# Performance work log

Measured on AMD Instinct MI355X. Metric: run time of the kernel, lower is better.

Reference implementation:

```python
import jax, jax.numpy as jnp
import numpy as np

N_NODES = 100000
N_EDGES = 1600000


def setup_inputs() -> dict:
    key = jax.random.key(0)
    k1, k2, k3, k4, k5, k6 = jax.random.split(key, 6)
    x = jax.random.normal(k1, (N_NODES, 2), dtype=jnp.float32)
    edge_index = jax.random.randint(k2, (2, N_EDGES), 0, N_NODES, dtype=jnp.int64)
    # Glorot-style init for GCN weights, zeros for biases (PyG defaults)
    W1 = jax.random.normal(k3, (2, 64), dtype=jnp.float32) * (1.0 / np.sqrt(2.0))
    b1 = jnp.zeros((64,), dtype=jnp.float32)
    W2 = jax.random.normal(k4, (64, 1), dtype=jnp.float32) * (1.0 / np.sqrt(64.0))
    b2 = jnp.zeros((1,), dtype=jnp.float32)
    return {"x": x, "edge_index": edge_index, "W1": W1, "b1": b1, "W2": W2, "b2": b2}


def reference(x, edge_index, W1, b1, W2, b2):
    N = x.shape[0]
    row, col = edge_index[0], edge_index[1]  # source, target (PyG flow source_to_target)
    # symmetric GCN normalization, degrees from target index (no self loops)
    deg = jax.ops.segment_sum(jnp.ones(edge_index.shape[1], x.dtype), col, num_segments=N)
    deg_inv_sqrt = jnp.where(deg > 0, jnp.where(deg > 0, deg, 1.0) ** -0.5, 0.0)
    norm = (deg_inv_sqrt[row] * deg_inv_sqrt[col])[:, None]  # [E,1]

    def gcn_conv(h, W, b):
        h = h @ W                       # [N,F_out] tiny GEMM
        msg = h[row] * norm             # gather + scale: [E,F_out]
        agg = jax.ops.segment_sum(msg, col, num_segments=N)  # scatter-add
        return agg + b

    h = jax.nn.relu(gcn_conv(x, W1, b1))   # dropout is identity in eval mode
    out = jax.nn.relu(gcn_conv(h, W2, b2))
    return out
```

## Files before the change

### kernel.cpp

```cpp
#include <hip/hip_runtime.h>
#include <math.h>

#define NN 100000
#define NE 1600000
#define BSHIFT 8
#define BKT 256
#define NB 391
#define NBP 392
#define EPB 4096
#define NPB 391
#define STRIDE 5120
#define RT 1024

__global__ void __launch_bounds__(RT) reorder_kernel(
        const int* __restrict__ row, const int* __restrict__ col,
        unsigned* __restrict__ cursor, unsigned* __restrict__ packed) {
    __shared__ int h[NBP], lb[NBP], gb[NBP];
    __shared__ int wsum[RT / 64];
    __shared__ unsigned st[EPB];
    __shared__ unsigned short sbkt[EPB];
    const int t = threadIdx.x;
    const int lane = t & 63, wid = t >> 6;
    const int e0 = blockIdx.x * EPB;
    const int n = min(EPB, NE - e0);

    for (int i = t; i < NBP; i += RT) h[i] = 0;
    __syncthreads();

    const int4* rv = (const int4*)(row + e0);
    const int4* cv = (const int4*)(col + e0);
    unsigned pk[4]; int bb[4];
#pragma unroll
    for (int u = 0; u < 4; ++u) bb[u] = -1;
    if (4 * t < n) {
        int4 r4 = rv[t], c4 = cv[t];
        int rr[4] = {r4.x, r4.y, r4.z, r4.w};
        int cc[4] = {c4.x, c4.y, c4.z, c4.w};
#pragma unroll
        for (int j = 0; j < 4; ++j) {
            pk[j] = ((unsigned)rr[j] << BSHIFT) | (unsigned)(cc[j] & (BKT - 1));
            bb[j] = cc[j] >> BSHIFT;
        }
    }
#pragma unroll
    for (int u = 0; u < 4; ++u)
        if (bb[u] >= 0) atomicAdd(&h[bb[u]], 1);
    __syncthreads();

    int v = (t < NBP) ? h[t] : 0;
    int incl = v;
#pragma unroll
    for (int d = 1; d < 64; d <<= 1) {
        int u = __shfl_up(incl, d);
        if (lane >= d) incl += u;
    }
    if (lane == 63) wsum[wid] = incl;
    __syncthreads();
    int off = 0;
#pragma unroll
    for (int j = 0; j < RT / 64 - 1; ++j)
        if (j < wid) off += wsum[j];
    if (t < NB) {
        lb[t] = off + incl - v;
        gb[t] = v ? (int)atomicAdd(&cursor[t], (unsigned)v) : 0;
    }
    __syncthreads();
    for (int i = t; i < NBP; i += RT) h[i] = 0;
    __syncthreads();

#pragma unroll
    for (int u = 0; u < 4; ++u) {
        if (bb[u] >= 0) {
            int r = atomicAdd(&h[bb[u]], 1);
            int idx = lb[bb[u]] + r;
            st[idx] = pk[u];
            sbkt[idx] = (unsigned short)bb[u];
        }
    }
    __syncthreads();
    for (int i = t; i < n; i += RT) {
        int b = sbkt[i];
        int pos = gb[b] + (i - lb[b]);
        if (pos < STRIDE)
            packed[b * STRIDE + pos] = st[i];
    }
}

__global__ void __launch_bounds__(RT) sortb_kernel(
        const unsigned* __restrict__ packed, const unsigned* __restrict__ cursor,
        const float2* __restrict__ x2,
        unsigned* __restrict__ srow, int2* __restrict__ node_rng,
        float* __restrict__ dis, float2* __restrict__ y2) {
    __shared__ int cnt[BKT], rk[BKT], sexA[BKT];
    __shared__ int wsum[RT / 64];
    __shared__ unsigned st[STRIDE];
    __shared__ unsigned srt[STRIDE];
    const int t = threadIdx.x;
    const int lane = t & 63, wid = t >> 6;
    const int b = blockIdx.x;
    const int s0 = b * STRIDE;
    const int L = min((int)cursor[b], STRIDE);
    const int L4 = L >> 2;

    if (t < BKT) { cnt[t] = 0; rk[t] = 0; }
    __syncthreads();

    const uint4* pv4 = (const uint4*)(packed + s0);
    for (int g = t; g < L4; g += RT) {
        uint4 p4 = pv4[g];
        ((uint4*)st)[g] = p4;
        atomicAdd(&cnt[p4.x & (BKT - 1u)], 1);
        atomicAdd(&cnt[p4.y & (BKT - 1u)], 1);
        atomicAdd(&cnt[p4.z & (BKT - 1u)], 1);
        atomicAdd(&cnt[p4.w & (BKT - 1u)], 1);
    }
    for (int i = 4 * L4 + t; i < L; i += RT) {
        unsigned p = packed[s0 + i];
        st[i] = p;
        atomicAdd(&cnt[p & (BKT - 1u)], 1);
    }
    __syncthreads();

    int v = (t < BKT) ? cnt[t] : 0;
    int incl = v;
#pragma unroll
    for (int d = 1; d < 64; d <<= 1) {
        int u = __shfl_up(incl, d);
        if (lane >= d) incl += u;
    }
    if (lane == 63 && wid < BKT / 64) wsum[wid] = incl;
    __syncthreads();
    int off = 0;
#pragma unroll
    for (int j = 0; j < BKT / 64 - 1; ++j)
        if (j < wid) off += wsum[j];
    if (t < BKT) {
        int sex = off + incl - v;
        sexA[t] = sex;
        int node = (b << BSHIFT) + t;
        if (node < NN) {
            float dv = (v > 0) ? rsqrtf((float)v) : 0.0f;
            dis[node] = dv;
            float2 xv = x2[node];
            y2[node] = make_float2(xv.x * dv, xv.y * dv);
            node_rng[node] = make_int2(s0 + sex, s0 + sex + v);
        }
    }
    __syncthreads();

    for (int i = t; i < L; i += RT) {
        unsigned p = st[i];
        int cl = p & (BKT - 1u);
        int r = atomicAdd(&rk[cl], 1);
        srt[sexA[cl] + r] = p >> BSHIFT;
    }
    __syncthreads();
    uint4* so4 = (uint4*)(srow + s0);
    for (int g = t; g < L4; g += RT) so4[g] = ((const uint4*)srt)[g];
    for (int i = 4 * L4 + t; i < L; i += RT) srow[s0 + i] = srt[i];
}

__global__ void conv1_kernel(const unsigned* __restrict__ srow, const int2* __restrict__ node_rng,
                             const float2* __restrict__ y2, const float* __restrict__ dis,
                             const float* __restrict__ W1, const float* __restrict__ b1,
                             const float* __restrict__ W2, float* __restrict__ z2) {
    __shared__ float sW0[64], sW1[64], sb1[64], sW2[64];
    int t = threadIdx.x;
    if (t < 64) { sW0[t] = W1[t]; sW1[t] = W1[64 + t]; sb1[t] = b1[t]; sW2[t] = W2[t]; }
    __syncthreads();
    int lane = t & 3;
    int node = blockIdx.x * 64 + (t >> 2);
    if (node >= NN) return;
    int2 rng = node_rng[node];
    float sx = 0.f, sy = 0.f;
    for (int k = rng.x + lane; k < rng.y; k += 4) {
        float2 v = y2[srow[k]];
        sx += v.x; sy += v.y;
    }
    sx += __shfl_xor(sx, 1); sy += __shfl_xor(sy, 1);
    sx += __shfl_xor(sx, 2); sy += __shfl_xor(sy, 2);
    float dv = dis[node];
    float a0 = sx * dv, a1 = sy * dv;
    float acc = 0.0f;
    int j0 = lane * 16;
#pragma unroll
    for (int jj = 0; jj < 16; ++jj) {
        int j = j0 + jj;
        float h = fmaf(a0, sW0[j], fmaf(a1, sW1[j], sb1[j]));
        acc = fmaf(fmaxf(h, 0.0f), sW2[j], acc);
    }
    acc += __shfl_xor(acc, 1);
    acc += __shfl_xor(acc, 2);
    if (lane == 0) z2[node] = acc * dv;
}

__global__ void conv2_kernel(const unsigned* __restrict__ srow, const int2* __restrict__ node_rng,
                             const float* __restrict__ z2, const float* __restrict__ dis,
                             const float* __restrict__ b2, float* __restrict__ out) {
    int t = threadIdx.x;
    int lane = t & 3;
    int node = blockIdx.x * 64 + (t >> 2);
    if (node >= NN) return;
    int2 rng = node_rng[node];
    float s = 0.f;
    for (int k = rng.x + lane; k < rng.y; k += 4)
        s += z2[srow[k]];
    s += __shfl_xor(s, 1);
    s += __shfl_xor(s, 2);
    if (lane == 0)
        out[node] = fmaxf(fmaf(dis[node], s, b2[0]), 0.0f);
}

extern "C" void kernel_launch(void* const* d_in, const int* in_sizes, int n_in,
                              void* d_out, int out_size, void* d_ws, size_t ws_size,
                              hipStream_t stream) {
    const float* x  = (const float*)d_in[0];
    const int*   ei = (const int*)d_in[1];
    const float* W1 = (const float*)d_in[2];
    const float* b1 = (const float*)d_in[3];
    const float* W2 = (const float*)d_in[4];
    const float* b2 = (const float*)d_in[5];
    float* out = (float*)d_out;

    const int* row = ei;
    const int* col = ei + NE;

    unsigned* packed   = (unsigned*)d_ws;
    unsigned* srow     = packed + (size_t)NB * STRIDE;
    float2*   y2       = (float2*)(srow + (size_t)NB * STRIDE);
    float*    dis      = (float*)(y2 + NN);
    float*    z2       = dis + NN;
    int2*     node_rng = (int2*)(z2 + NN);
    unsigned* cursor   = (unsigned*)(node_rng + NN);

    hipMemsetAsync(cursor, 0, NB * sizeof(unsigned), stream);

    reorder_kernel<<<NPB, RT, 0, stream>>>(row, col, cursor, packed);
    sortb_kernel  <<<NB, RT, 0, stream>>>(packed, cursor, (const float2*)x,
                                          srow, node_rng, dis, y2);
    conv1_kernel  <<<(NN + 63) / 64, 256, 0, stream>>>(srow, node_rng, y2, dis,
                                                       W1, b1, W2, z2);
    conv2_kernel  <<<(NN + 63) / 64, 256, 0, stream>>>(srow, node_rng, z2, dis, b2, out);
}
```

Before: 117.6 us.

## Use larger 448-node buckets, direct-address scatter staging, and re-read packed in sort

The bucket width grows from 256 to 448 nodes, which cuts the bucket count to 224. Each reorder block now handles 6400 edges with 8 per thread, and per-edge global addresses are precomputed into shared memory so the scatter pass writes directly. The sort kernel no longer stages packed data in LDS and instead re-reads it from global memory for the second pass. Together these aim to reduce block count, per-block fixed overhead and LDS pressure, at the cost of integer division, larger shared arrays and a second global read.

```diff
diff --git a/kernel.cpp b/kernel.cpp
--- a/kernel.cpp
+++ b/kernel.cpp
@@ -3,86 +3,90 @@
 
 #define NN 100000
 #define NE 1600000
-#define BSHIFT 8
-#define BKT 256
-#define NB 391
-#define NBP 392
-#define EPB 4096
-#define NPB 391
-#define STRIDE 5120
+#define BKT 448
+#define NB 224
+#define EPB 6400
+#define NPB 250
+#define STRIDE 8192
 #define RT 1024
 
 __global__ void __launch_bounds__(RT) reorder_kernel(
         const int* __restrict__ row, const int* __restrict__ col,
         unsigned* __restrict__ cursor, unsigned* __restrict__ packed) {
-    __shared__ int h[NBP], lb[NBP], gb[NBP];
+    __shared__ int h[NB], lb[NB];
+    __shared__ unsigned gaddr[NB], glim[NB];
     __shared__ int wsum[RT / 64];
-    __shared__ unsigned st[EPB];
-    __shared__ unsigned short sbkt[EPB];
+    __shared__ uint2 sga[EPB];
     const int t = threadIdx.x;
     const int lane = t & 63, wid = t >> 6;
     const int e0 = blockIdx.x * EPB;
-    const int n = min(EPB, NE - e0);
-
-    for (int i = t; i < NBP; i += RT) h[i] = 0;
+
+    for (int i = t; i < NB; i += RT) h[i] = 0;
     __syncthreads();
 
     const int4* rv = (const int4*)(row + e0);
     const int4* cv = (const int4*)(col + e0);
-    unsigned pk[4]; int bb[4];
-#pragma unroll
-    for (int u = 0; u < 4; ++u) bb[u] = -1;
-    if (4 * t < n) {
-        int4 r4 = rv[t], c4 = cv[t];
-        int rr[4] = {r4.x, r4.y, r4.z, r4.w};
-        int cc[4] = {c4.x, c4.y, c4.z, c4.w};
-#pragma unroll
-        for (int j = 0; j < 4; ++j) {
-            pk[j] = ((unsigned)rr[j] << BSHIFT) | (unsigned)(cc[j] & (BKT - 1));
-            bb[j] = cc[j] >> BSHIFT;
-        }
-    }
-#pragma unroll
-    for (int u = 0; u < 4; ++u)
+    unsigned pk[8]; int bb[8];
+#pragma unroll
+    for (int u = 0; u < 8; ++u) bb[u] = -1;
+#pragma unroll
+    for (int g = 0; g < 2; ++g) {
+        int grp = g * RT + t;
+        if (grp < EPB / 4) {
+            int4 r4 = rv[grp], c4 = cv[grp];
+            int rr[4] = {r4.x, r4.y, r4.z, r4.w};
+            int cc[4] = {c4.x, c4.y, c4.z, c4.w};
+#pragma unroll
+            for (int j = 0; j < 4; ++j) {
+                int b = cc[j] / BKT;
+                int cl = cc[j] - b * BKT;
+                pk[4 * g + j] = ((unsigned)rr[j] << 9) | (unsigned)cl;
+                bb[4 * g + j] = b;
+            }
+        }
+    }
+#pragma unroll
+    for (int u = 0; u < 8; ++u)
         if (bb[u] >= 0) atomicAdd(&h[bb[u]], 1);
     __syncthreads();
 
-    int v = (t < NBP) ? h[t] : 0;
+    int v = (t < NB) ? h[t] : 0;
     int incl = v;
 #pragma unroll
     for (int d = 1; d < 64; d <<= 1) {
-        int u = __shfl_up(incl, d);
-        if (lane >= d) incl += u;
+        int u2 = __shfl_up(incl, d);
+        if (lane >= d) incl += u2;
     }
     if (lane == 63) wsum[wid] = incl;
     __syncthreads();
     int off = 0;
 #pragma unroll
-    for (int j = 0; j < RT / 64 - 1; ++j)
+    for (int j = 0; j < 3; ++j)
         if (j < wid) off += wsum[j];
     if (t < NB) {
         lb[t] = off + incl - v;
-        gb[t] = v ? (int)atomicAdd(&cursor[t], (unsigned)v) : 0;
-    }
-    __syncthreads();
-    for (int i = t; i < NBP; i += RT) h[i] = 0;
-    __syncthreads();
-
-#pragma unroll
-    for (int u = 0; u < 4; ++u) {
+        unsigned base = v ? atomicAdd(&cursor[t], (unsigned)v) : 0u;
+        gaddr[t] = (unsigned)t * STRIDE + base;
+        glim[t]  = (unsigned)(t + 1) * STRIDE;
+    }
+    __syncthreads();
+    for (int i = t; i < NB; i += RT) h[i] = 0;
+    __syncthreads();
+
+#pragma unroll
+    for (int u = 0; u < 8; ++u) {
         if (bb[u] >= 0) {
-            int r = atomicAdd(&h[bb[u]], 1);
-            int idx = lb[bb[u]] + r;
-            st[idx] = pk[u];
-            sbkt[idx] = (unsigned short)bb[u];
-        }
-    }
-    __syncthreads();
-    for (int i = t; i < n; i += RT) {
-        int b = sbkt[i];
-        int pos = gb[b] + (i - lb[b]);
-        if (pos < STRIDE)
-            packed[b * STRIDE + pos] = st[i];
+            int b = bb[u];
+            int r = atomicAdd(&h[b], 1);
+            unsigned a = gaddr[b] + (unsigned)r;
+            if (a >= glim[b]) a = 0xFFFFFFFFu;
+            sga[lb[b] + r] = make_uint2(pk[u], a);
+        }
+    }
+    __syncthreads();
+    for (int i = t; i < EPB; i += RT) {
+        uint2 e = sga[i];
+        if (e.y != 0xFFFFFFFFu) packed[e.y] = e.x;
     }
 }
 
@@ -92,67 +96,72 @@
         unsigned* __restrict__ srow, int2* __restrict__ node_rng,
         float* __restrict__ dis, float2* __restrict__ y2) {
     __shared__ int cnt[BKT], rk[BKT], sexA[BKT];
-    __shared__ int wsum[RT / 64];
-    __shared__ unsigned st[STRIDE];
+    __shared__ int wsum[(BKT + 63) / 64];
     __shared__ unsigned srt[STRIDE];
     const int t = threadIdx.x;
     const int lane = t & 63, wid = t >> 6;
     const int b = blockIdx.x;
-    const int s0 = b * STRIDE;
+    const unsigned s0 = (unsigned)b * STRIDE;
     const int L = min((int)cursor[b], STRIDE);
     const int L4 = L >> 2;
 
-    if (t < BKT) { cnt[t] = 0; rk[t] = 0; }
+    for (int i = t; i < BKT; i += RT) { cnt[i] = 0; rk[i] = 0; }
     __syncthreads();
 
     const uint4* pv4 = (const uint4*)(packed + s0);
     for (int g = t; g < L4; g += RT) {
         uint4 p4 = pv4[g];
-        ((uint4*)st)[g] = p4;
-        atomicAdd(&cnt[p4.x & (BKT - 1u)], 1);
-        atomicAdd(&cnt[p4.y & (BKT - 1u)], 1);
-        atomicAdd(&cnt[p4.z & (BKT - 1u)], 1);
-        atomicAdd(&cnt[p4.w & (BKT - 1u)], 1);
-    }
-    for (int i = 4 * L4 + t; i < L; i += RT) {
-        unsigned p = packed[s0 + i];
-        st[i] = p;
-        atomicAdd(&cnt[p & (BKT - 1u)], 1);
-    }
+        atomicAdd(&cnt[p4.x & 511u], 1);
+        atomicAdd(&cnt[p4.y & 511u], 1);
+        atomicAdd(&cnt[p4.z & 511u], 1);
+        atomicAdd(&cnt[p4.w & 511u], 1);
+    }
+    for (int i = 4 * L4 + t; i < L; i += RT)
+        atomicAdd(&cnt[packed[s0 + i] & 511u], 1);
     __syncthreads();
 
     int v = (t < BKT) ? cnt[t] : 0;
     int incl = v;
 #pragma unroll
     for (int d = 1; d < 64; d <<= 1) {
-        int u = __shfl_up(incl, d);
-        if (lane >= d) incl += u;
-    }
-    if (lane == 63 && wid < BKT / 64) wsum[wid] = incl;
+        int u2 = __shfl_up(incl, d);
+        if (lane >= d) incl += u2;
+    }
+    if (lane == 63 && wid < (BKT + 63) / 64) wsum[wid] = incl;
     __syncthreads();
     int off = 0;
 #pragma unroll
-    for (int j = 0; j < BKT / 64 - 1; ++j)
+    for (int j = 0; j < (BKT + 63) / 64 - 1; ++j)
         if (j < wid) off += wsum[j];
     if (t < BKT) {
         int sex = off + incl - v;
         sexA[t] = sex;
-        int node = (b << BSHIFT) + t;
+        int node = b * BKT + t;
         if (node < NN) {
             float dv = (v > 0) ? rsqrtf((float)v) : 0.0f;
             dis[node] = dv;
             float2 xv = x2[node];
             y2[node] = make_float2(xv.x * dv, xv.y * dv);
-            node_rng[node] = make_int2(s0 + sex, s0 + sex + v);
-        }
-    }
-    __syncthreads();
-
-    for (int i = t; i < L; i += RT) {
-        unsigned p = st[i];
-        int cl = p & (BKT - 1u);
+            node_rng[node] = make_int2((int)(s0 + sex), (int)(s0 + sex + v));
+        }
+    }
+    __syncthreads();
+
+    for (int g = t; g < L4; g += RT) {
+        uint4 p4 = pv4[g];
+        unsigned pp[4] = {p4.x, p4.y, p4.z, p4.w};
+#pragma unroll
+        for (int j = 0; j < 4; ++j) {
+            int cl = pp[j] & 511u;
+            int r = atomicAdd(&rk[cl], 1);
+            srt[sexA[cl] + r] = pp[j] >> 9;
+        }
+    }
+    for (int i = 4 * L4 + t; i < L; i += RT) {
+        unsigned p = packed[s0 + i];
+        int cl = p & 511u;
         int r = atomicAdd(&rk[cl], 1);
-        srt[sexA[cl] + r] = p >> BSHIFT;
+        srt[sexA[cl] + r] = p >> 9;
     }
     __syncthreads();
     uint4* so4 = (uint4*)(srow + s0);
```

Measured after the change: 111.8 us. 4.9% less time.
